# Performance work log

Hardware: AMD Instinct MI355X
Metric: run time of the kernel (lower is better)

The kernel has to match this reference:

```python
import jax, jax.numpy as jnp
import numpy as np

N_EXPERTS = 8
D_MODEL = 1024
D_FFN = 4096
BATCH, SEQ = 4, 1024


def setup_inputs() -> dict:
    key = jax.random.key(0)
    ks = jax.random.split(key, 12)
    T = BATCH * SEQ
    s_d = 1.0 / np.sqrt(D_MODEL)
    s_f = 1.0 / np.sqrt(D_FFN)
    return {
        "x": jax.random.normal(ks[0], (BATCH, SEQ, D_MODEL), jnp.float32),
        "noise": jax.random.normal(ks[1], (T, N_EXPERTS), jnp.float32),
        # router (torch Linear stored as [out,in]; we store pre-transposed [in,out])
        "Wg": jax.random.uniform(ks[2], (D_MODEL, N_EXPERTS), jnp.float32, -s_d, s_d),
        "bg": jax.random.uniform(ks[3], (N_EXPERTS,), jnp.float32, -s_d, s_d),
        "Wn": jax.random.uniform(ks[4], (D_MODEL, N_EXPERTS), jnp.float32, -s_d, s_d),
        "bn": jax.random.uniform(ks[5], (N_EXPERTS,), jnp.float32, -s_d, s_d),
        # stacked expert weights: fc1 [E, D, F], fc2 [E, F, D]
        "W1": jax.random.uniform(ks[6], (N_EXPERTS, D_MODEL, D_FFN), jnp.float32, -s_d, s_d),
        "b1": jax.random.uniform(ks[7], (N_EXPERTS, D_FFN), jnp.float32, -s_d, s_d),
        "W2": jax.random.uniform(ks[8], (N_EXPERTS, D_FFN, D_MODEL), jnp.float32, -s_f, s_f),
        "b2": jax.random.uniform(ks[9], (N_EXPERTS, D_MODEL), jnp.float32, -s_f, s_f),
        "top_k": 2,
    }


def reference(x, noise, Wg, bg, Wn, bn, W1, b1, W2, b2, top_k):
    B, S, D = x.shape
    xf = x.reshape(-1, D)                       # [T, D]
    T = xf.shape[0]
    # --- noisy top-k router ---
    logits = xf @ Wg + bg                       # [T, E]
    noise_logits = xf @ Wn + bn                 # [T, E]
    noisy = logits + noise * jax.nn.softplus(noise_logits)
    top_v, top_i = jax.lax.top_k(noisy, top_k)  # [T, k]
    sparse = jnp.full_like(noisy, -jnp.inf)
    sparse = sparse.at[jnp.arange(T)[:, None], top_i].set(top_v)
    gates = jax.nn.softmax(sparse, axis=-1)     # [T, E], zeros off top-k
    # --- experts (dense grouped GEMM; non-selected tokens zeroed by gates) ---
    h = jax.nn.relu(jnp.einsum('td,edf->etf', xf, W1) + b1[:, None, :])  # [E, T, F]
    eo = jnp.einsum('etf,efd->etd', h, W2) + b2[:, None, :]              # [E, T, D]
    out = jnp.einsum('etd,te->td', eo, gates)                            # [T, D]
    return out.reshape(B, S, D)
```

## Files before the change

kernel.cpp:

```cpp
#include <hip/hip_runtime.h>
#include <math.h>

#define T_TOK 4096
#define DM 1024
#define DF 4096
#define NE 8

#define BM 128
#define BN 128
#define BK 64

typedef __attribute__((ext_vector_type(8))) short bf16x8;
typedef __attribute__((ext_vector_type(4))) float f32x4;
typedef unsigned long long u64;

__device__ __forceinline__ unsigned short f2bf(float f) {
    union { float f; unsigned int u; } v; v.f = f;
    unsigned int r = v.u + 0x7FFFu + ((v.u >> 16) & 1u);
    return (unsigned short)(r >> 16);
}

__device__ __forceinline__ void glds16(const void* g, void* l) {
    __builtin_amdgcn_global_load_lds(
        (const __attribute__((address_space(1))) unsigned int*)g,
        (__attribute__((address_space(3))) unsigned int*)l, 16, 0, 0);
}

__global__ __launch_bounds__(256) void k_router(
    const float* __restrict__ x, const float* __restrict__ noise,
    const float* __restrict__ Wg, const float* __restrict__ bg,
    const float* __restrict__ Wn, const float* __restrict__ bn,
    int* __restrict__ counts, int* __restrict__ slots, float* __restrict__ gates)
{
    const int lane = threadIdx.x & 63;
    const int wave = threadIdx.x >> 6;
    const int t = blockIdx.x * 4 + wave;
    const float* xr = x + (size_t)t * DM + lane * 16;

    float accg[8], accn[8];
    #pragma unroll
    for (int i = 0; i < 8; ++i) { accg[i] = 0.f; accn[i] = 0.f; }

    #pragma unroll
    for (int dd = 0; dd < 16; ++dd) {
        float xv = xr[dd];
        int d = lane * 16 + dd;
        float4 g0 = *(const float4*)(Wg + d * 8);
        float4 g1 = *(const float4*)(Wg + d * 8 + 4);
        float4 n0 = *(const float4*)(Wn + d * 8);
        float4 n1 = *(const float4*)(Wn + d * 8 + 4);
        accg[0] += xv * g0.x; accg[1] += xv * g0.y; accg[2] += xv * g0.z; accg[3] += xv * g0.w;
        accg[4] += xv * g1.x; accg[5] += xv * g1.y; accg[6] += xv * g1.z; accg[7] += xv * g1.w;
        accn[0] += xv * n0.x; accn[1] += xv * n0.y; accn[2] += xv * n0.z; accn[3] += xv * n0.w;
        accn[4] += xv * n1.x; accn[5] += xv * n1.y; accn[6] += xv * n1.z; accn[7] += xv * n1.w;
    }
    #pragma unroll
    for (int s = 1; s < 64; s <<= 1) {
        #pragma unroll
        for (int e = 0; e < 8; ++e) {
            accg[e] += __shfl_xor(accg[e], s, 64);
            accn[e] += __shfl_xor(accn[e], s, 64);
        }
    }
    if (lane == 0) {
        float nv[8];
        #pragma unroll
        for (int e = 0; e < 8; ++e) {
            float lg = accg[e] + bg[e];
            float nl = accn[e] + bn[e];
            float sp = (nl > 20.f) ? nl : log1pf(expf(nl));
            nv[e] = lg + noise[(size_t)t * NE + e] * sp;
        }
        int i0 = 0;
        #pragma unroll
        for (int e = 1; e < 8; ++e) if (nv[e] > nv[i0]) i0 = e;
        int i1 = -1;
        #pragma unroll
        for (int e = 0; e < 8; ++e) {
            if (e == i0) continue;
            if (i1 < 0 || nv[e] > nv[i1]) i1 = e;
        }
        float ex = expf(nv[i1] - nv[i0]);
        float g0 = 1.f / (1.f + ex);
        float g1 = ex / (1.f + ex);
        int p0 = atomicAdd(counts + i0, 1);
        slots[i0 * T_TOK + p0] = t * 2;     gates[i0 * T_TOK + p0] = g0;
        int p1 = atomicAdd(counts + i1, 1);
        slots[i1 * T_TOK + p1] = t * 2 + 1; gates[i1 * T_TOK + p1] = g1;
    }
}

__global__ __launch_bounds__(256) void k_xcast(const float* __restrict__ x,
                                               unsigned short* __restrict__ xb)
{
    int i = blockIdx.x * 256 + threadIdx.x;
    float4 v = ((const float4*)x)[i];
    u64 p = (u64)f2bf(v.x) | ((u64)f2bf(v.y) << 16) | ((u64)f2bf(v.z) << 32) | ((u64)f2bf(v.w) << 48);
    ((u64*)xb)[i] = p;
}

__global__ __launch_bounds__(256) void k_tr(const float* __restrict__ in,
                                            unsigned short* __restrict__ out,
                                            int R, int C)
{
    __shared__ unsigned short t[64 * 68];
    const int e = blockIdx.z;
    const int C0 = blockIdx.x * 64, R0 = blockIdx.y * 64;
    const float* ip = in + ((size_t)e * R + R0) * C + C0;
    unsigned short* op = out + ((size_t)e * C + C0) * R + R0;
    const int tid = threadIdx.x;

    #pragma unroll
    for (int p = 0; p < 4; ++p) {
        int r = p * 16 + (tid >> 4), c4 = (tid & 15) * 4;
        float4 v = *(const float4*)(ip + (size_t)r * C + c4);
        t[(c4 + 0) * 68 + r] = f2bf(v.x);
        t[(c4 + 1) * 68 + r] = f2bf(v.y);
        t[(c4 + 2) * 68 + r] = f2bf(v.z);
        t[(c4 + 3) * 68 + r] = f2bf(v.w);
    }
    __syncthreads();
    #pragma unroll
    for (int p = 0; p < 4; ++p) {
        int c = p * 16 + (tid >> 4), r4 = (tid & 15) * 4;
        u64 v = *(const u64*)(t + c * 68 + r4);
        *(u64*)(op + (size_t)c * R + r4) = v;
    }
}

__global__ __launch_bounds__(256) void k_fc1(
    const unsigned short* __restrict__ xb, const unsigned short* __restrict__ W1t,
    const float* __restrict__ b1, const int* __restrict__ counts,
    const int* __restrict__ slots, unsigned short* __restrict__ h)
{
    const int e = blockIdx.z;
    const int cnt = counts[e];
    const int mt = blockIdx.y;
    if (mt * BM >= cnt) return;
    const int nb = blockIdx.x * BN;

    __shared__ unsigned short As[BM * BK];
    __shared__ unsigned short Bs[BN * BK];
    __shared__ int slot_s[BM];

    const int tid = threadIdx.x;
    if (tid < BM) {
        int gi = mt * BM + tid;
        slot_s[tid] = (gi < cnt) ? slots[e * T_TOK + gi] : -1;
    }
    __syncthreads();

    const int lane = tid & 63, wv = tid >> 6;
    const int wm = (wv & 1) * 64, wn = (wv >> 1) * 64;
    const int ml = lane & 15, kg = lane >> 4;

    const int srow = tid >> 3;
    const int cg = (tid & 7) ^ (srow & 7);

    const unsigned short* ag[4];
    const unsigned short* bg[4];
    const unsigned short* wbase = W1t + (size_t)e * DF * DM;
    #pragma unroll
    for (int c = 0; c < 4; ++c) {
        int row = c * 32 + srow;
        int s = slot_s[row];
        int tok = (s >= 0) ? (s >> 1) : 0;
        ag[c] = xb + (size_t)tok * DM + cg * 8;
        bg[c] = wbase + (size_t)(nb + row) * DM + cg * 8;
    }
    unsigned short* al = As + wv * 512;
    unsigned short* bl = Bs + wv * 512;

    f32x4 acc[4][4];
    #pragma unroll
    for (int ni = 0; ni < 4; ++ni)
        #pragma unroll
        for (int mi = 0; mi < 4; ++mi) acc[ni][mi] = (f32x4){0.f, 0.f, 0.f, 0.f};

    for (int k0 = 0; k0 < DM; k0 += BK) {
        #pragma unroll
        for (int c = 0; c < 4; ++c) glds16(ag[c] + k0, al + c * 2048);
        #pragma unroll
        for (int c = 0; c < 4; ++c) glds16(bg[c] + k0, bl + c * 2048);
        __syncthreads();
        #pragma unroll
        for (int ks = 0; ks < 2; ++ks) {
            const int ch = (((ks * 4 + kg) ^ (ml & 7)) << 3);
            bf16x8 af[4], bf[4];
            #pragma unroll
            for (int mi = 0; mi < 4; ++mi)
                af[mi] = *(const bf16x8*)(As + (wm + mi * 16 + ml) * BK + ch);
            #pragma unroll
            for (int ni = 0; ni < 4; ++ni)
                bf[ni] = *(const bf16x8*)(Bs + (wn + ni * 16 + ml) * BK + ch);
            #pragma unroll
            for (int ni = 0; ni < 4; ++ni)
                #pragma unroll
                for (int mi = 0; mi < 4; ++mi)
                    acc[ni][mi] = __builtin_amdgcn_mfma_f32_16x16x32_bf16(bf[ni], af[mi], acc[ni][mi], 0, 0, 0);
        }
        __syncthreads();
    }

    #pragma unroll
    for (int mi = 0; mi < 4; ++mi) {
        int s = slot_s[wm + mi * 16 + ml];
        if (s < 0) continue;
        #pragma unroll
        for (int ni = 0; ni < 4; ++ni) {
            int n0 = wn + ni * 16 + kg * 4;
            float4 bb = *(const float4*)(b1 + (size_t)e * DF + nb + n0);
            float v0 = fmaxf(acc[ni][mi][0] + bb.x, 0.f);
            float v1 = fmaxf(acc[ni][mi][1] + bb.y, 0.f);
            float v2 = fmaxf(acc[ni][mi][2] + bb.z, 0.f);
            float v3 = fmaxf(acc[ni][mi][3] + bb.w, 0.f);
            u64 p = (u64)f2bf(v0) | ((u64)f2bf(v1) << 16) | ((u64)f2bf(v2) << 32) | ((u64)f2bf(v3) << 48);
            *(u64*)(h + (size_t)s * DF + nb + n0) = p;
        }
    }
}

__global__ __launch_bounds__(256) void k_fc2(
    const unsigned short* __restrict__ h, const unsigned short* __restrict__ W2t,
    const float* __restrict__ b2, const int* __restrict__ counts,
    const int* __restrict__ slots, const float* __restrict__ gates,
    float* __restrict__ out)
{
    const int e = blockIdx.z >> 1;
    const int kz = blockIdx.z & 1;
    const int cnt = counts[e];
    const int mt = blockIdx.y;
    if (mt * BM >= cnt) return;
    const int nb = blockIdx.x * BN;

    __shared__ unsigned short As[BM * BK];
    __shared__ unsigned short Bs[BN * BK];
    __shared__ int slot_s[BM];
    __shared__ float gate_s[BM];

    const int tid = threadIdx.x;
    if (tid < BM) {
        int gi = mt * BM + tid;
        if (gi < cnt) {
            slot_s[tid] = slots[e * T_TOK + gi];
            gate_s[tid] = gates[e * T_TOK + gi];
        } else { slot_s[tid] = -1; gate_s[tid] = 0.f; }
    }
    __syncthreads();

    const int lane = tid & 63, wv = tid >> 6;
    const int wm = (wv & 1) * 64, wn = (wv >> 1) * 64;
    const int ml = lane & 15, kg = lane >> 4;

    const int srow = tid >> 3;
    const int cg = (tid & 7) ^ (srow & 7);

    const unsigned short* ag[4];
    const unsigned short* bg[4];
    const unsigned short* wbase = W2t + (size_t)e * DM * DF;
    #pragma unroll
    for (int c = 0; c < 4; ++c) {
        int row = c * 32 + srow;
        int s = slot_s[row];
        int sl = (s >= 0) ? s : 0;
        ag[c] = h + (size_t)sl * DF + cg * 8;
        bg[c] = wbase + (size_t)(nb + row) * DF + cg * 8;
    }
    unsigned short* al = As + wv * 512;
    unsigned short* bl = Bs + wv * 512;

    f32x4 acc[4][4];
    #pragma unroll
    for (int ni = 0; ni < 4; ++ni)
        #pragma unroll
        for (int mi = 0; mi < 4; ++mi) acc[ni][mi] = (f32x4){0.f, 0.f, 0.f, 0.f};

    const int kbeg = kz * (DF / 2), kend = kbeg + DF / 2;
    for (int k0 = kbeg; k0 < kend; k0 += BK) {
        #pragma unroll
        for (int c = 0; c < 4; ++c) glds16(ag[c] + k0, al + c * 2048);
        #pragma unroll
        for (int c = 0; c < 4; ++c) glds16(bg[c] + k0, bl + c * 2048);
        __syncthreads();
        #pragma unroll
        for (int ks = 0; ks < 2; ++ks) {
            const int ch = (((ks * 4 + kg) ^ (ml & 7)) << 3);
            bf16x8 af[4], bf[4];
            #pragma unroll
            for (int mi = 0; mi < 4; ++mi)
                af[mi] = *(const bf16x8*)(As + (wm + mi * 16 + ml) * BK + ch);
            #pragma unroll
            for (int ni = 0; ni < 4; ++ni)
                bf[ni] = *(const bf16x8*)(Bs + (wn + ni * 16 + ml) * BK + ch);
            #pragma unroll
            for (int ni = 0; ni < 4; ++ni)
                #pragma unroll
                for (int mi = 0; mi < 4; ++mi)
                    acc[ni][mi] = __builtin_amdgcn_mfma_f32_16x16x32_bf16(bf[ni], af[mi], acc[ni][mi], 0, 0, 0);
        }
        __syncthreads();
    }

    #pragma unroll
    for (int mi = 0; mi < 4; ++mi) {
        int s = slot_s[wm + mi * 16 + ml];
        if (s < 0) continue;
        float g = gate_s[wm + mi * 16 + ml];
        float* orow = out + (size_t)(s >> 1) * DM + nb;
        #pragma unroll
        for (int ni = 0; ni < 4; ++ni) {
            int n0 = wn + ni * 16 + kg * 4;
            float4 bb;
            if (kz == 0) bb = *(const float4*)(b2 + (size_t)e * DM + nb + n0);
            else         bb = make_float4(0.f, 0.f, 0.f, 0.f);
            atomicAdd(orow + n0 + 0, g * (acc[ni][mi][0] + bb.x));
            atomicAdd(orow + n0 + 1, g * (acc[ni][mi][1] + bb.y));
            atomicAdd(orow + n0 + 2, g * (acc[ni][mi][2] + bb.z));
            atomicAdd(orow + n0 + 3, g * (acc[ni][mi][3] + bb.w));
        }
    }
}

extern "C" void kernel_launch(void* const* d_in, const int* in_sizes, int n_in,
                              void* d_out, int out_size, void* d_ws, size_t ws_size,
                              hipStream_t stream) {
    const float* x     = (const float*)d_in[0];
    const float* noise = (const float*)d_in[1];
    const float* Wg    = (const float*)d_in[2];
    const float* bg    = (const float*)d_in[3];
    const float* Wn    = (const float*)d_in[4];
    const float* bn    = (const float*)d_in[5];
    const float* W1    = (const float*)d_in[6];
    const float* b1    = (const float*)d_in[7];
    const float* W2    = (const float*)d_in[8];
    const float* b2    = (const float*)d_in[9];
    float* out = (float*)d_out;

    char* ws = (char*)d_ws;
    int*   counts = (int*)ws;
    int*   slots  = (int*)(ws + 4096);
    float* gates  = (float*)(ws + 4096 + NE * T_TOK * 4);
    unsigned short* xb = (unsigned short*)(ws + 4096 + 2 * NE * T_TOK * 4);
    unsigned short* hh = xb + (size_t)T_TOK * DM;
    unsigned short* Wt = hh + (size_t)2 * T_TOK * DF;

    hipMemsetAsync(counts, 0, 4096, stream);
    hipMemsetAsync(out, 0, (size_t)out_size * sizeof(float), stream);

    k_router<<<T_TOK / 4, 256, 0, stream>>>(x, noise, Wg, bg, Wn, bn, counts, slots, gates);
    k_xcast<<<T_TOK * DM / 1024, 256, 0, stream>>>(x, xb);

    k_tr<<<dim3(DF / 64, DM / 64, NE), 256, 0, stream>>>(W1, Wt, DM, DF);
    k_fc1<<<dim3(DF / BN, T_TOK / BM, NE), 256, 0, stream>>>(xb, Wt, b1, counts, slots, hh);

    k_tr<<<dim3(DM / 64, DF / 64, NE), 256, 0, stream>>>(W2, Wt, DF, DM);
    k_fc2<<<dim3(DM / BN, T_TOK / BM, NE * 2), 256, 0, stream>>>(hh, Wt, b2, counts, slots, gates, out);
}
```

Before: 823.6 us.

## Double-buffer expert GEMMs, reorder grid, replace fc2 atomics with combine kernel

```diff
diff --git a/kernel.cpp b/kernel.cpp
--- a/kernel.cpp
+++ b/kernel.cpp
@@ -8,7 +8,7 @@
 
 #define BM 128
 #define BN 128
-#define BK 64
+#define BK 32
 
 typedef __attribute__((ext_vector_type(8))) short bf16x8;
 typedef __attribute__((ext_vector_type(4))) float f32x4;
@@ -18,6 +18,10 @@
     union { float f; unsigned int u; } v; v.f = f;
     unsigned int r = v.u + 0x7FFFu + ((v.u >> 16) & 1u);
     return (unsigned short)(r >> 16);
+}
+__device__ __forceinline__ float bf2f(unsigned short u) {
+    union { float f; unsigned int u; } v; v.u = ((unsigned int)u) << 16;
+    return v.f;
 }
 
 __device__ __forceinline__ void glds16(const void* g, void* l) {
@@ -128,19 +132,19 @@
     }
 }
 
-__global__ __launch_bounds__(256) void k_fc1(
+__global__ __launch_bounds__(256, 4) void k_fc1(
     const unsigned short* __restrict__ xb, const unsigned short* __restrict__ W1t,
     const float* __restrict__ b1, const int* __restrict__ counts,
     const int* __restrict__ slots, unsigned short* __restrict__ h)
 {
-    const int e = blockIdx.z;
+    const int e = blockIdx.x;
     const int cnt = counts[e];
-    const int mt = blockIdx.y;
+    const int mt = blockIdx.z;
     if (mt * BM >= cnt) return;
-    const int nb = blockIdx.x * BN;
-
-    __shared__ unsigned short As[BM * BK];
-    __shared__ unsigned short Bs[BN * BK];
+    const int nb = blockIdx.y * BN;
+
+    __shared__ unsigned short As[2][BM * BK];
+    __shared__ unsigned short Bs[2][BN * BK];
     __shared__ int slot_s[BM];
 
     const int tid = threadIdx.x;
@@ -150,26 +154,26 @@
     }
     __syncthreads();
 
+    const int srow = tid >> 2;
+    const int cg = (tid & 3) ^ ((tid >> 3) & 3);
+
+    const unsigned short* ag[2];
+    const unsigned short* bgp[2];
+    const unsigned short* wbase = W1t + (size_t)e * DF * DM;
+    #pragma unroll
+    for (int c = 0; c < 2; ++c) {
+        int row = c * 64 + srow;
+        int s = slot_s[row];
+        int tok = (s >= 0) ? (s >> 1) : 0;
+        ag[c]  = xb + (size_t)tok * DM + cg * 8;
+        bgp[c] = wbase + (size_t)(nb + row) * DM + cg * 8;
+    }
+
     const int lane = tid & 63, wv = tid >> 6;
     const int wm = (wv & 1) * 64, wn = (wv >> 1) * 64;
     const int ml = lane & 15, kg = lane >> 4;
-
-    const int srow = tid >> 3;
-    const int cg = (tid & 7) ^ (srow & 7);
-
-    const unsigned short* ag[4];
-    const unsigned short* bg[4];
-    const unsigned short* wbase = W1t + (size_t)e * DF * DM;
-    #pragma unroll
-    for (int c = 0; c < 4; ++c) {
-        int row = c * 32 + srow;
-        int s = slot_s[row];
-        int tok = (s >= 0) ? (s >> 1) : 0;
-        ag[c] = xb + (size_t)tok * DM + cg * 8;
-        bg[c] = wbase + (size_t)(nb + row) * DM + cg * 8;
-    }
-    unsigned short* al = As + wv * 512;
-    unsigned short* bl = Bs + wv * 512;
+    const int rch = (kg ^ ((ml >> 1) & 3)) * 8;
+    const int lo = wv * 512;
 
     f32x4 acc[4][4];
     #pragma unroll
@@ -177,29 +181,33 @@
         #pragma unroll
         for (int mi = 0; mi < 4; ++mi) acc[ni][mi] = (f32x4){0.f, 0.f, 0.f, 0.f};
 
+    #pragma unroll
+    for (int c = 0; c < 2; ++c) glds16(ag[c],  &As[0][c * 2048 + lo]);
+    #pragma unroll
+    for (int c = 0; c < 2; ++c) glds16(bgp[c], &Bs[0][c * 2048 + lo]);
+
+    int buf = 0;
     for (int k0 = 0; k0 < DM; k0 += BK) {
-        #pragma unroll
-        for (int c = 0; c < 4; ++c) glds16(ag[c] + k0, al + c * 2048);
-        #pragma unroll
-        for (int c = 0; c < 4; ++c) glds16(bg[c] + k0, bl + c * 2048);
         __syncthreads();
-        #pragma unroll
-        for (int ks = 0; ks < 2; ++ks) {
-            const int ch = (((ks * 4 + kg) ^ (ml & 7)) << 3);
-            bf16x8 af[4], bf[4];
+        if (k0 + BK < DM) {
+            #pragma unroll
+            for (int c = 0; c < 2; ++c) glds16(ag[c] + k0 + BK,  &As[buf ^ 1][c * 2048 + lo]);
+            #pragma unroll
+            for (int c = 0; c < 2; ++c) glds16(bgp[c] + k0 + BK, &Bs[buf ^ 1][c * 2048 + lo]);
+        }
+        bf16x8 af[4], bfr[4];
+        #pragma unroll
+        for (int mi = 0; mi < 4; ++mi)
+            af[mi] = *(const bf16x8*)(&As[buf][(wm + mi * 16 + ml) * BK + rch]);
+        #pragma unroll
+        for (int ni = 0; ni < 4; ++ni)
+            bfr[ni] = *(const bf16x8*)(&Bs[buf][(wn + ni * 16 + ml) * BK + rch]);
+        #pragma unroll
+        for (int ni = 0; ni < 4; ++ni)
             #pragma unroll
             for (int mi = 0; mi < 4; ++mi)
-                af[mi] = *(const bf16x8*)(As + (wm + mi * 16 + ml) * BK + ch);
-            #pragma unroll
-            for (int ni = 0; ni < 4; ++ni)
-                bf[ni] = *(const bf16x8*)(Bs + (wn + ni * 16 + ml) * BK + ch);
-            #pragma unroll
-            for (int ni = 0; ni < 4; ++ni)
-                #pragma unroll
-                for (int mi = 0; mi < 4; ++mi)
-                    acc[ni][mi] = __builtin_amdgcn_mfma_f32_16x16x32_bf16(bf[ni], af[mi], acc[ni][mi], 0, 0, 0);
-        }
-        __syncthreads();
+                acc[ni][mi] = __builtin_amdgcn_mfma_f32_16x16x32_bf16(bfr[ni], af[mi], acc[ni][mi], 0, 0, 0);
+        buf ^= 1;
     }
 
     #pragma unroll
@@ -220,21 +228,21 @@
     }
 }
 
-__global__ __launch_bounds__(256) void k_fc2(
+__global__ __launch_bounds__(256, 4) void k_fc2(
     const unsigned short* __restrict__ h, const unsigned short* __restrict__ W2t,
     const float* __restrict__ b2, const int* __restrict__ counts,
     const int* __restrict__ slots, const float* __restrict__ gates,
-    float* __restrict__ out)
-{
-    const int e = blockIdx.z >> 1;
+    unsigned short* __restrict__ eo)
+{
+    const int e = blockIdx.x;
+    const int cnt = counts[e];
+    const int mt = blockIdx.z >> 1;
     const int kz = blockIdx.z & 1;
-    const int cnt = counts[e];
-    const int mt = blockIdx.y;
     if (mt * BM >= cnt) return;
-    const int nb = blockIdx.x * BN;
-
-    __shared__ unsigned short As[BM * BK];
-    __shared__ unsigned short Bs[BN * BK];
+    const int nb = blockIdx.y * BN;
+
+    __shared__ unsigned short As[2][BM * BK];
+    __shared__ unsigned short Bs[2][BN * BK];
     __shared__ int slot_s[BM];
     __shared__ float gate_s[BM];
 
@@ -248,26 +256,27 @@
     }
     __syncthreads();
 
+    const int srow = tid >> 2;
+    const int cg = (tid & 3) ^ ((tid >> 3) & 3);
+    const int kbeg = kz * (DF / 2);
+
+    const unsigned short* ag[2];
+    const unsigned short* bgp[2];
+    const unsigned short* wbase = W2t + (size_t)e * DM * DF;
+    #pragma unroll
+    for (int c = 0; c < 2; ++c) {
+        int row = c * 64 + srow;
+        int s = slot_s[row];
+        int sl = (s >= 0) ? s : 0;
+        ag[c]  = h + (size_t)sl * DF + kbeg + cg * 8;
+        bgp[c] = wbase + (size_t)(nb + row) * DF + kbeg + cg * 8;
+    }
+
     const int lane = tid & 63, wv = tid >> 6;
     const int wm = (wv & 1) * 64, wn = (wv >> 1) * 64;
     const int ml = lane & 15, kg = lane >> 4;
-
-    const int srow = tid >> 3;
-    const int cg = (tid & 7) ^ (srow & 7);
-
-    const unsigned short* ag[4];
-    const unsigned short* bg[4];
-    const unsigned short* wbase = W2t + (size_t)e * DM * DF;
-    #pragma unroll
-    for (int c = 0; c < 4; ++c) {
-        int row = c * 32 + srow;
-        int s = slot_s[row];
-        int sl = (s >= 0) ? s : 0;
-        ag[c] = h + (size_t)sl * DF + cg * 8;
-        bg[c] = wbase + (size_t)(nb + row) * DF + cg * 8;
-    }
-    unsigned short* al = As + wv * 512;
-    unsigned short* bl = Bs + wv * 512;
+    const int rch = (kg ^ ((ml >> 1) & 3)) * 8;
+    const int lo = wv * 512;
 
     f32x4 acc[4][4];
     #pragma unroll
@@ -275,50 +284,77 @@
         #pragma unroll
         for (int mi = 0; mi < 4; ++mi) acc[ni][mi] = (f32x4){0.f, 0.f, 0.f, 0.f};
 
-    const int kbeg = kz * (DF / 2), kend = kbeg + DF / 2;
-    for (int k0 = kbeg; k0 < kend; k0 += BK) {
-        #pragma unroll
-        for (int c = 0; c < 4; ++c) glds16(ag[c] + k0, al + c * 2048);
-        #pragma unroll
-        for (int c = 0; c < 4; ++c) glds16(bg[c] + k0, bl + c * 2048);
+    #pragma unroll
+    for (int c = 0; c < 2; ++c) glds16(ag[c],  &As[0][c * 2048 + lo]);
+    #pragma unroll
+    for (int c = 0; c < 2; ++c) glds16(bgp[c], &Bs[0][c * 2048 + lo]);
+
+    int buf = 0;
+    for (int k0 = 0; k0 < DF / 2; k0 += BK) {
         __syncthreads();
-        #pragma unroll
-        for (int ks = 0; ks < 2; ++ks) {
-            const int ch = (((ks * 4 + kg) ^ (ml & 7)) << 3);
-            bf16x8 af[4], bf[4];
+        if (k0 + BK < DF / 2) {
+            #pragma unroll
+            for (int c = 0; c < 2; ++c) glds16(ag[c] + k0 + BK,  &As[buf ^ 1][c * 2048 + lo]);
+            #pragma unroll
+            for (int c = 0; c < 2; ++c) glds16(bgp[c] + k0 + BK, &Bs[buf ^ 1][c * 2048 + lo]);
+        }
+        bf16x8 af[4], bfr[4];
+        #pragma unroll
+        for (int mi = 0; mi < 4; ++mi)
+            af[mi] = *(const bf16x8*)(&As[buf][(wm + mi * 16 + ml) * BK + rch]);
+        #pragma unroll
+        for (int ni = 0; ni < 4; ++ni)
+            bfr[ni] = *(const bf16x8*)(&Bs[buf][(wn + ni * 16 + ml) * BK + rch]);
+        #pragma unroll
+        for (int ni = 0; ni < 4; ++ni)
             #pragma unroll
             for (int mi = 0; mi < 4; ++mi)
-                af[mi] = *(const bf16x8*)(As + (wm + mi * 16 + ml) * BK + ch);
-            #pragma unroll
-            for (int ni = 0; ni < 4; ++ni)
-                bf[ni] = *(const bf16x8*)(Bs + (wn + ni * 16 + ml) * BK + ch);
-            #pragma unroll
-            for (int ni = 0; ni < 4; ++ni)
-                #pragma unroll
-                for (int mi = 0; mi < 4; ++mi)
-                    acc[ni][mi] = __builtin_amdgcn_mfma_f32_16x16x32_bf16(bf[ni], af[mi], acc[ni][mi], 0, 0, 0);
-        }
-        __syncthreads();
-    }
-
+                acc[ni][mi] = __builtin_amdgcn_mfma_f32_16x16x32_bf16(bfr[ni], af[mi], acc[ni][mi], 0, 0, 0);
+        buf ^= 1;
+    }
+
+    unsigned short* eob = eo + (size_t)kz * 2 * T_TOK * DM;
     #pragma unroll
     for (int mi = 0; mi < 4; ++mi) {
         int s = slot_s[wm + mi * 16 + ml];
         if (s < 0) continue;
         float g = gate_s[wm + mi * 16 + ml];
-        float* orow = out + (size_t)(s >> 1) * DM + nb;
         #pragma unroll
         for (int ni = 0; ni < 4; ++ni) {
             int n0 = wn + ni * 16 + kg * 4;
             float4 bb;
             if (kz == 0) bb = *(const float4*)(b2 + (size_t)e * DM + nb + n0);
             else         bb = make_float4(0.f, 0.f, 0.f, 0.f);
-            atomicAdd(orow + n0 + 0, g * (acc[ni][mi][0] + bb.x));
-            atomicAdd(orow + n0 + 1, g * (acc[ni][mi][1] + bb.y));
-            atomicAdd(orow + n0 + 2, g * (acc[ni][mi][2] + bb.z));
-            atomicAdd(orow + n0 + 3, g * (acc[ni][mi][3] + bb.w));
-        }
-    }
+            float v0 = g * (acc[ni][mi][0] + bb.x);
+            float v1 = g * (acc[ni][mi][1] + bb.y);
+            float v2 = g * (acc[ni][mi][2] + bb.z);
+            float v3 = g * (acc[ni][mi][3] + bb.w);
+            u64 p = (u64)f2bf(v0) | ((u64)f2bf(v1) << 16) | ((u64)f2bf(v2) << 32) | ((u64)f2bf(v3) << 48);
+            *(u64*)(eob + (size_t)s * DM + nb + n0) = p;
+        }
+    }
+}
+
+__global__ __launch_bounds__(256) void k_comb(const unsigned short* __restrict__ eo,
+                                              float* __restrict__ out)
+{
+    int i = blockIdx.x * 256 + threadIdx.x;
+    int t = i >> 8;
+    int d4 = (i & 255) * 4;
+    const unsigned short* p0 = eo + (size_t)(2 * t) * DM + d4;
+    const unsigned short* p1 = p0 + DM;
+    const unsigned short* q0 = p0 + (size_t)2 * T_TOK * DM;
+    const unsigned short* q1 = q0 + DM;
+    ushort4 a0 = *(const ushort4*)p0;
+    ushort4 a1 = *(const ushort4*)p1;
+    ushort4 b0 = *(const ushort4*)q0;
+    ushort4 b1 = *(const ushort4*)q1;
+    float4 r;
+    r.x = bf2f(a0.x) + bf2f(a1.x) + bf2f(b0.x) + bf2f(b1.x);
+    r.y = bf2f(a0.y) + bf2f(a1.y) + bf2f(b0.y) + bf2f(b1.y);
+    r.z = bf2f(a0.z) + bf2f(a1.z) + bf2f(b0.z) + bf2f(b1.z);
+    r.w = bf2f(a0.w) + bf2f(a1.w) + bf2f(b0.w) + bf2f(b1.w);
+    ((float4*)out)[i] = r;
 }
 
 extern "C" void kernel_launch(void* const* d_in, const int* in_sizes, int n_in,
@@ -343,16 +379,18 @@
     unsigned short* xb = (unsigned short*)(ws + 4096 + 2 * NE * T_TOK * 4);
     unsigned short* hh = xb + (size_t)T_TOK * DM;
     unsigned short* Wt = hh + (size_t)2 * T_TOK * DF;
+    unsigned short* eo = Wt + (size_t)NE * DM * DF;
 
     hipMemsetAsync(counts, 0, 4096, stream);
-    hipMemsetAsync(out, 0, (size_t)out_size * sizeof(float), stream);
 
     k_router<<<T_TOK / 4, 256, 0, stream>>>(x, noise, Wg, bg, Wn, bn, counts, slots, gates);
     k_xcast<<<T_TOK * DM / 1024, 256, 0, stream>>>(x, xb);
 
     k_tr<<<dim3(DF / 64, DM / 64, NE), 256, 0, stream>>>(W1, Wt, DM, DF);
-    k_fc1<<<dim3(DF / BN, T_TOK / BM, NE), 256, 0, stream>>>(xb, Wt, b1, counts, slots, hh);
+    k_fc1<<<dim3(NE, DF / BN, T_TOK / BM), 256, 0, stream>>>(xb, Wt, b1, counts, slots, hh);
 
     k_tr<<<dim3(DM / 64, DF / 64, NE), 256, 0, stream>>>(W2, Wt, DF, DM);
-    k_fc2<<<dim3(DM / BN, T_TOK / BM, NE * 2), 256, 0, stream>>>(hh, Wt, b2, counts, slots, gates, out);
-}
+    k_fc2<<<dim3(NE, DM / BN, (T_TOK / BM) * 2), 256, 0, stream>>>(hh, Wt, b2, counts, slots, gates, eo);
+
+    k_comb<<<T_TOK * DM / 1024, 256, 0, stream>>>(eo, out);
+}
```

Measured after the change: 670.1 us. -18.6%, faster.
